# Performance work log

Measured on AMD Instinct MI355X. Metric: run time of the kernel, lower is better.

Reference implementation:

```python
import jax, jax.numpy as jnp
import numpy as np

V, OOV, E, HE, HD, B, S, T = 50000, 100, 128, 256, 256, 32, 256, 16
NEG = -1e20


def lstm(x, W, U, b, h0, c0):
    # x: [B, L, F]; standard (Keras-style i,f,g,o) LSTM via scan over time
    def step(carry, xt):
        h, c = carry
        z = xt @ W + h @ U + b
        i, f, g, o = jnp.split(z, 4, axis=-1)
        c = jax.nn.sigmoid(f) * c + jax.nn.sigmoid(i) * jnp.tanh(g)
        h = jax.nn.sigmoid(o) * jnp.tanh(c)
        return (h, c), h
    (h, c), hs = jax.lax.scan(step, (h0, c0), jnp.swapaxes(x, 0, 1))
    return jnp.swapaxes(hs, 0, 1), h, c


def setup_inputs() -> dict:
    key = jax.random.key(0)
    ks = jax.random.split(key, 16)
    g = lambda i, shape: jax.random.normal(ks[i], shape, dtype=jnp.float32) * 0.05
    return {
        'x': jax.random.randint(ks[0], (B, S), 0, V),
        'x_with_oov': jax.random.randint(ks[1], (B, S), 0, V + OOV),
        'x_len': jax.random.randint(ks[2], (B,), 1, S + 1),
        'dec_x': jax.random.randint(ks[3], (B, T), 0, V),
        'embedding': g(4, (V, E)),
        'Wenc': g(5, (E, 4 * HE)), 'Uenc': g(6, (HE, 4 * HE)), 'benc': jnp.zeros(4 * HE, jnp.float32),
        'We2d': g(7, (HE, HD)), 'be2d': jnp.zeros(HD, jnp.float32),
        'Wdec': g(8, (E, 4 * HD)), 'Udec': g(9, (HD, 4 * HD)), 'bdec': jnp.zeros(4 * HD, jnp.float32),
        'Wattn': g(10, (HD, HE)),
        'Wout': g(11, (HE + HD, HD)), 'bout': jnp.zeros(HD, jnp.float32),
        'Wgen': g(12, (HD, V)),
        'Wcopy': g(13, (HE, HD)), 'bcopy': jnp.zeros(HD, jnp.float32),
    }


def reference(x, x_with_oov, x_len, dec_x, embedding, Wenc, Uenc, benc,
              We2d, be2d, Wdec, Udec, bdec, Wattn, Wout, bout, Wgen, Wcopy, bcopy):
    # Encoder (unidirectional; Keras encoder ignores mask in this branch)
    enc_out, eh, ec = lstm(embedding[x], Wenc, Uenc, benc,
                           jnp.zeros((B, HE), embedding.dtype), jnp.zeros((B, HE), embedding.dtype))
    # NOTE: source applies encoder2decoder_state to BOTH h and c (faithful)
    h0 = eh @ We2d + be2d
    c0 = ec @ We2d + be2d
    # Decoder LSTM
    dec_out, sh, sc = lstm(embedding[dec_x], Wdec, Udec, bdec, h0, c0)  # [B,T,HD]
    mask = jnp.arange(S)[None, :] < x_len[:, None]                      # [B,S]
    # Attention (score_mode='general')
    scores = jnp.einsum('bth,he,bse->bts', dec_out, Wattn, enc_out)     # [B,T,S]
    scores = jnp.where(mask[:, None, :], scores, NEG)
    aw = jax.nn.softmax(scores, axis=2)
    ctx = jnp.einsum('bts,bse->bte', aw, enc_out)                       # [B,T,HE]
    attn_out = jnp.tanh(jnp.concatenate([ctx, dec_out], axis=-1) @ Wout + bout)  # [B,T,HD]
    # Generation scores, padded with tiny constant over OOV slots
    gen = jnp.exp(attn_out @ Wgen)                                      # [B,T,V]
    gen = jnp.pad(gen, ((0, 0), (0, 0), (0, OOV)), constant_values=1e-10)
    # Copy scores over source positions, scattered into extended vocab
    copy_seq = jnp.einsum('bsh,bth->bts', jnp.tanh(enc_out @ Wcopy + bcopy), attn_out)
    copy_seq = jnp.exp(jnp.where(mask[:, None, :], copy_seq, NEG))      # [B,T,S]
    b_idx = jnp.arange(B)[:, None, None]
    t_idx = jnp.arange(T)[None, :, None]
    v_idx = x_with_oov[:, None, :]                                      # broadcast to [B,T,S]
    copy_vocab = jnp.zeros((B, T, V + OOV), gen.dtype).at[b_idx, t_idx, v_idx].add(copy_seq)
    total = gen + copy_vocab
    log_prob = jnp.log(total / jnp.sum(total, axis=2, keepdims=True))
    return log_prob, sh, sc
```

## Files before the change

### kernel.cpp

```cpp
#include <hip/hip_runtime.h>

#define V_   50000
#define OOV_ 100
#define VO_  50100
#define E_   128
#define HE_  256
#define HD_  256
#define B_   32
#define S_   256
#define T_   16

typedef _Float16 h2_t __attribute__((ext_vector_type(2)));
typedef __attribute__((ext_vector_type(8))) short bfrag_t;
typedef __attribute__((ext_vector_type(4))) float f32x4;

union U32H2 { unsigned u; h2_t h; };
union FRAG  { uint4 u; bfrag_t s; };

static __device__ __forceinline__ float bf2f(unsigned short b) {
  return __uint_as_float(((unsigned)b) << 16);
}
static __device__ __forceinline__ unsigned short f2bf(float f) {
  unsigned u = __float_as_uint(f);
  unsigned r = (u + 0x7fffu + ((u >> 16) & 1u)) >> 16;
  return (unsigned short)r;
}
static __device__ __forceinline__ unsigned pk2bf(float a, float b) {
  return ((unsigned)f2bf(b) << 16) | (unsigned)f2bf(a);
}
static __device__ __forceinline__ float sigm(float x) { return 1.f / (1.f + expf(-x)); }

static __device__ __forceinline__ float dot2u(unsigned upair, unsigned hpairv, float acc) {
  U32H2 a; a.u = upair;
  U32H2 b; b.u = hpairv;
#if __has_builtin(__builtin_amdgcn_fdot2)
  return __builtin_amdgcn_fdot2(a.h, b.h, acc, false);
#else
  acc = fmaf((float)a.h.x, (float)b.h.x, acc);
  return fmaf((float)a.h.y, (float)b.h.y, acc);
#endif
}

__global__ __launch_bounds__(256) void gemm_f32(
    const float* __restrict__ A, const float* __restrict__ Bw,
    const float* __restrict__ bias, float* __restrict__ C,
    int M, int N, int K, int ldC, int act)
{
  __shared__ float As[16][64];
  __shared__ float Bs[16][64];
  const int tid = threadIdx.x;
  const int tx = tid & 15, ty = tid >> 4;
  const int row0 = blockIdx.y * 64, col0 = blockIdx.x * 64;
  float acc[4][4] = {{0.f}};
  for (int k0 = 0; k0 < K; k0 += 16) {
#pragma unroll
    for (int q = 0; q < 4; q++) {
      int idx = q * 256 + tid;
      int m = idx >> 4, kk = idx & 15;
      As[kk][m] = A[(size_t)(row0 + m) * K + (k0 + kk)];
      int k2 = idx >> 6, n = idx & 63;
      int cc = col0 + n;
      Bs[k2][n] = (cc < N) ? Bw[(size_t)(k0 + k2) * N + cc] : 0.f;
    }
    __syncthreads();
#pragma unroll
    for (int kk = 0; kk < 16; kk++) {
      float4 a4 = *(const float4*)&As[kk][ty * 4];
      float4 b4 = *(const float4*)&Bs[kk][tx * 4];
      float av[4] = {a4.x, a4.y, a4.z, a4.w};
      float bv[4] = {b4.x, b4.y, b4.z, b4.w};
#pragma unroll
      for (int i = 0; i < 4; i++)
#pragma unroll
        for (int j = 0; j < 4; j++)
          acc[i][j] = fmaf(av[i], bv[j], acc[i][j]);
    }
    __syncthreads();
  }
#pragma unroll
  for (int i = 0; i < 4; i++) {
    int r = row0 + ty * 4 + i;
#pragma unroll
    for (int j = 0; j < 4; j++) {
      int c = col0 + tx * 4 + j;
      if (c < N) {
        float v = acc[i][j] + (bias ? bias[c] : 0.f);
        if (act == 1) v = tanhf(v);
        else if (act == 2) v = expf(v);
        C[(size_t)r * ldC + c] = v;
      }
    }
  }
}

#define DOT8(u0, u1, hpi)                \
  acc[0] = dot2u(u0.x, hpi, acc[0]);     \
  acc[1] = dot2u(u0.y, hpi, acc[1]);     \
  acc[2] = dot2u(u0.z, hpi, acc[2]);     \
  acc[3] = dot2u(u0.w, hpi, acc[3]);     \
  acc[4] = dot2u(u1.x, hpi, acc[4]);     \
  acc[5] = dot2u(u1.y, hpi, acc[5]);     \
  acc[6] = dot2u(u1.z, hpi, acc[6]);     \
  acc[7] = dot2u(u1.w, hpi, acc[7]);

__global__ __launch_bounds__(1024) void lstm_rec2(
    const float* __restrict__ Xpre, const unsigned* __restrict__ Upk2,
    const float* __restrict__ h0, const float* __restrict__ c0,
    float* __restrict__ outH, float* __restrict__ hN, float* __restrict__ cN,
    int steps)
{
  __shared__ unsigned ldsU[32 * 1028];
  __shared__ float zpart[4 * 1028];
  __shared__ unsigned hpair[128];
  const int tid = threadIdx.x, b = blockIdx.x;
  const int jg = tid >> 3, kq = tid & 7;

  uint4 Ur[24];
  const unsigned* ubase = Upk2 + jg * 8;
#pragma unroll
  for (int i = 0; i < 12; i++) {
    int p = kq * 16 + i;
    Ur[2 * i]     = *(const uint4*)(ubase + p * 1024);
    Ur[2 * i + 1] = *(const uint4*)(ubase + p * 1024 + 4);
  }
#pragma unroll
  for (int i = 0; i < 4; i++) {
    int p = kq * 16 + 12 + i;
    uint4 q0 = *(const uint4*)(ubase + p * 1024);
    uint4 q1 = *(const uint4*)(ubase + p * 1024 + 4);
    *(uint4*)&ldsU[(kq * 4 + i) * 1028 + jg * 8] = q0;
    *(uint4*)&ldsU[(kq * 4 + i) * 1028 + jg * 8 + 4] = q1;
  }
  float c = 0.f, hcur = 0.f;
  if (tid < 256) {
    c    = c0 ? c0[b * 256 + tid] : 0.f;
    hcur = h0 ? h0[b * 256 + tid] : 0.f;
  }
  if (tid < 128) {
    float a  = h0 ? h0[b * 256 + 2 * tid] : 0.f;
    float b2 = h0 ? h0[b * 256 + 2 * tid + 1] : 0.f;
    U32H2 cv; cv.h = h2_t{(_Float16)a, (_Float16)b2};
    hpair[tid] = cv.u;
  }
  __syncthreads();

  const float* xp = Xpre + (size_t)b * steps * 1024;
  const unsigned* myld = &ldsU[kq * 4 * 1028 + jg * 8];

  for (int t = 0; t < steps; t++) {
    float x0 = 0.f, x1 = 0.f, x2 = 0.f, x3 = 0.f;
    if (tid < 256) {
      x0 = xp[t * 1024 + tid];
      x1 = xp[t * 1024 + 256 + tid];
      x2 = xp[t * 1024 + 512 + tid];
      x3 = xp[t * 1024 + 768 + tid];
    }
    float acc[8] = {0.f, 0.f, 0.f, 0.f, 0.f, 0.f, 0.f, 0.f};
    {
      uint4 hA = *(const uint4*)&hpair[kq * 16];
      DOT8(Ur[0], Ur[1], hA.x)  DOT8(Ur[2], Ur[3], hA.y)
      DOT8(Ur[4], Ur[5], hA.z)  DOT8(Ur[6], Ur[7], hA.w)
    }
    {
      uint4 hB = *(const uint4*)&hpair[kq * 16 + 4];
      DOT8(Ur[8], Ur[9], hB.x)   DOT8(Ur[10], Ur[11], hB.y)
      DOT8(Ur[12], Ur[13], hB.z) DOT8(Ur[14], Ur[15], hB.w)
    }
    {
      uint4 hC = *(const uint4*)&hpair[kq * 16 + 8];
      DOT8(Ur[16], Ur[17], hC.x) DOT8(Ur[18], Ur[19], hC.y)
      DOT8(Ur[20], Ur[21], hC.z) DOT8(Ur[22], Ur[23], hC.w)
    }
    {
      uint4 hD = *(const uint4*)&hpair[kq * 16 + 12];
      unsigned hh[4] = {hD.x, hD.y, hD.z, hD.w};
#pragma unroll
      for (int r = 0; r < 4; r++) {
        uint4 u0 = *(const uint4*)(myld + r * 1028);
        uint4 u1 = *(const uint4*)(myld + r * 1028 + 4);
        unsigned hpi = hh[r];
        DOT8(u0, u1, hpi)
      }
    }
#pragma unroll
    for (int g = 0; g < 8; g++) acc[g] += __shfl_xor(acc[g], 1);
    if ((kq & 1) == 0) {
      int r = kq >> 1;
      *(float4*)&zpart[r * 1028 + jg * 8]     = make_float4(acc[0], acc[1], acc[2], acc[3]);
      *(float4*)&zpart[r * 1028 + jg * 8 + 4] = make_float4(acc[4], acc[5], acc[6], acc[7]);
    }
    __syncthreads();
    if (tid < 256) {
      int j = tid;
      float s0 = 0.f, s1 = 0.f, s2 = 0.f, s3 = 0.f;
#pragma unroll
      for (int r = 0; r < 4; r++) {
        s0 += zpart[r * 1028 + j];
        s1 += zpart[r * 1028 + 256 + j];
        s2 += zpart[r * 1028 + 512 + j];
        s3 += zpart[r * 1028 + 768 + j];
      }
      float zi = x0 + s0, zf = x1 + s1, zg = x2 + s2, zo = x3 + s3;
      c = sigm(zf) * c + sigm(zi) * tanhf(zg);
      hcur = sigm(zo) * tanhf(c);
      outH[((size_t)b * steps + t) * 256 + j] = hcur;
      float hother = __shfl_xor(hcur, 1);
      if ((j & 1) == 0) {
        U32H2 cv; cv.h = h2_t{(_Float16)hcur, (_Float16)hother};
        hpair[j >> 1] = cv.u;
      }
    }
    __syncthreads();
  }
  if (tid < 256) {
    hN[b * 256 + tid] = hcur;
    cN[b * 256 + tid] = c;
  }
}

__global__ __launch_bounds__(256) void gen_mfma(
    const unsigned short* __restrict__ Abf, const float* __restrict__ Wgen,
    float* __restrict__ out)
{
  const int w = threadIdx.x >> 6, lane = threadIdx.x & 63;
  const int m0 = blockIdx.y * 64 + w * 16;
  const int n0 = blockIdx.x * 64;
  const int l16 = lane & 15, lq = lane >> 4;
  f32x4 acc[4] = {f32x4{0,0,0,0}, f32x4{0,0,0,0}, f32x4{0,0,0,0}, f32x4{0,0,0,0}};
  for (int k0 = 0; k0 < 256; k0 += 32) {
    FRAG a;
    a.u = *(const uint4*)(Abf + (size_t)(m0 + l16) * 256 + k0 + lq * 8);
#pragma unroll
    for (int ns = 0; ns < 4; ns++) {
      int n = n0 + ns * 16 + l16;
      int nc = n < V_ ? n : V_ - 1;
      const float* bp = Wgen + (size_t)(k0 + lq * 8) * V_ + nc;
      FRAG bf;
      bf.u.x = pk2bf(bp[0],          bp[(size_t)V_]);
      bf.u.y = pk2bf(bp[2 * (size_t)V_], bp[3 * (size_t)V_]);
      bf.u.z = pk2bf(bp[4 * (size_t)V_], bp[5 * (size_t)V_]);
      bf.u.w = pk2bf(bp[6 * (size_t)V_], bp[7 * (size_t)V_]);
      acc[ns] = __builtin_amdgcn_mfma_f32_16x16x32_bf16(a.s, bf.s, acc[ns], 0, 0, 0);
    }
  }
#pragma unroll
  for (int ns = 0; ns < 4; ns++) {
    int col = n0 + ns * 16 + l16;
    if (col < V_) {
#pragma unroll
      for (int r = 0; r < 4; r++) {
        int row = m0 + lq * 4 + r;
        out[(size_t)row * VO_ + col] = expf(acc[ns][r]);
      }
    }
  }
}

__global__ __launch_bounds__(256) void attn_kernel(
    const float* __restrict__ dq, const float* __restrict__ enc,
    const int* __restrict__ x_len, float* __restrict__ ctx)
{
  __shared__ float q[256];
  __shared__ float eb[32][256];
  __shared__ float sc[256];
  __shared__ float red[8];
  const int bt = blockIdx.x, tid = threadIdx.x;
  const int b = bt >> 4;
  q[tid] = dq[(size_t)bt * 256 + tid];
  const int len = x_len[b];
  const float* encb = enc + (size_t)b * S_ * 256;
  __syncthreads();
  const int s_loc = tid >> 3, hb = (tid & 7) * 32;
  for (int cch = 0; cch < 8; cch++) {
#pragma unroll
    for (int qq = 0; qq < 32; qq++) {
      int idx = qq * 256 + tid;
      eb[idx >> 8][idx & 255] = encb[(size_t)(cch * 32) * 256 + idx];
    }
    __syncthreads();
    float p = 0.f;
#pragma unroll
    for (int h = 0; h < 32; h++) p = fmaf(q[hb + h], eb[s_loc][hb + h], p);
    p += __shfl_down(p, 4, 8);
    p += __shfl_down(p, 2, 8);
    p += __shfl_down(p, 1, 8);
    if ((tid & 7) == 0) sc[cch * 32 + s_loc] = p;
    __syncthreads();
  }
  float my = (tid < len) ? sc[tid] : -1e30f;
  float m = my;
#pragma unroll
  for (int o = 32; o >= 1; o >>= 1) m = fmaxf(m, __shfl_xor(m, o));
  if ((tid & 63) == 0) red[tid >> 6] = m;
  __syncthreads();
  float bm = fmaxf(fmaxf(red[0], red[1]), fmaxf(red[2], red[3]));
  float e = expf(my - bm);
  float s = e;
#pragma unroll
  for (int o = 32; o >= 1; o >>= 1) s += __shfl_xor(s, o);
  if ((tid & 63) == 0) red[4 + (tid >> 6)] = s;
  __syncthreads();
  float tot = red[4] + red[5] + red[6] + red[7];
  sc[tid] = e / tot;
  __syncthreads();
  float acc = 0.f;
  for (int s2 = 0; s2 < 256; s2++) acc = fmaf(sc[s2], encb[(size_t)s2 * 256 + tid], acc);
  ctx[(size_t)bt * 256 + tid] = acc;
}

__global__ __launch_bounds__(256) void copyseq_kernel(
    const float* __restrict__ at, const float* __restrict__ cp,
    const int* __restrict__ x_len, float* __restrict__ cseq)
{
  __shared__ float q[256];
  __shared__ float eb[32][256];
  __shared__ float sc[256];
  const int bt = blockIdx.x, tid = threadIdx.x;
  const int b = bt >> 4;
  q[tid] = at[(size_t)bt * 256 + tid];
  const int len = x_len[b];
  const float* cpb = cp + (size_t)b * S_ * 256;
  __syncthreads();
  const int s_loc = tid >> 3, hb = (tid & 7) * 32;
  for (int cch = 0; cch < 8; cch++) {
#pragma unroll
    for (int qq = 0; qq < 32; qq++) {
      int idx = qq * 256 + tid;
      eb[idx >> 8][idx & 255] = cpb[(size_t)(cch * 32) * 256 + idx];
    }
    __syncthreads();
    float p = 0.f;
#pragma unroll
    for (int h = 0; h < 32; h++) p = fmaf(q[hb + h], eb[s_loc][hb + h], p);
    p += __shfl_down(p, 4, 8);
    p += __shfl_down(p, 2, 8);
    p += __shfl_down(p, 1, 8);
    if ((tid & 7) == 0) sc[cch * 32 + s_loc] = p;
    __syncthreads();
  }
  cseq[(size_t)bt * 256 + tid] = (tid < len) ? expf(sc[tid]) : 0.f;
}

__global__ void embed_kernel(const int* __restrict__ idx, const float* __restrict__ emb,
                             float* __restrict__ out) {
  int r = blockIdx.x;
  out[(size_t)r * E_ + threadIdx.x] = emb[(size_t)idx[r] * E_ + threadIdx.x];
}
__global__ void packU2_kernel(const float* __restrict__ U, unsigned* __restrict__ out) {
  int i = blockIdx.x * 256 + threadIdx.x;
  int p = i >> 10, col = i & 1023;
  float a = U[(size_t)(2 * p) * 1024 + col];
  float b = U[(size_t)(2 * p + 1) * 1024 + col];
  U32H2 cv; cv.h = h2_t{(_Float16)a, (_Float16)b};
  out[i] = cv.u;
}
__global__ void f2bf_kernel(const float* __restrict__ in, unsigned short* __restrict__ out, int n) {
  int i = blockIdx.x * 256 + threadIdx.x;
  if (i < n) out[i] = f2bf(in[i]);
}
__global__ void concat_kernel(const float* __restrict__ ctx, const float* __restrict__ dec,
                              float* __restrict__ cat) {
  int i = blockIdx.x * 256 + threadIdx.x;
  int r = i >> 9, j = i & 511;
  cat[i] = (j < 256) ? ctx[r * 256 + j] : dec[r * 256 + (j - 256)];
}
__global__ void pad_kernel(float* __restrict__ out) {
  int i = blockIdx.x * 256 + threadIdx.x;
  if (i < B_ * T_ * OOV_) {
    int bt = i / OOV_, j = i - bt * OOV_;
    out[(size_t)bt * VO_ + V_ + j] = 1e-10f;
  }
}
__global__ void scatter_kernel(const float* __restrict__ cseq, const int* __restrict__ xoov,
                               float* __restrict__ out) {
  int i = blockIdx.x * 256 + threadIdx.x;
  int bt = i >> 8, s = i & 255, b = bt >> 4;
  float v = cseq[i];
  if (v != 0.f) atomicAdd(&out[(size_t)bt * VO_ + xoov[b * S_ + s]], v);
}
__global__ __launch_bounds__(256) void rowsum_kernel(const float* __restrict__ out,
                                                     float* __restrict__ rowlog) {
  __shared__ float red[256];
  int bt = blockIdx.x, tid = threadIdx.x;
  const float* row = out + (size_t)bt * VO_;
  float s = 0.f;
  for (int i = tid; i < VO_; i += 256) s += row[i];
  red[tid] = s;
  __syncthreads();
  for (int o = 128; o >= 1; o >>= 1) {
    if (tid < o) red[tid] += red[tid + o];
    __syncthreads();
  }
  if (tid == 0) rowlog[bt] = logf(red[0]);
}
__global__ void finalize_kernel(float* __restrict__ out, const float* __restrict__ rowlog) {
  size_t i = (size_t)blockIdx.x * 256 + threadIdx.x;
  if (i < (size_t)B_ * T_ * VO_) {
    int bt = (int)(i / VO_);
    out[i] = logf(out[i]) - rowlog[bt];
  }
}

extern "C" void kernel_launch(void* const* d_in, const int* in_sizes, int n_in,
                              void* d_out, int out_size, void* d_ws, size_t ws_size,
                              hipStream_t stream) {
  const int*   x     = (const int*)d_in[0];
  const int*   xoov  = (const int*)d_in[1];
  const int*   xlen  = (const int*)d_in[2];
  const int*   decx  = (const int*)d_in[3];
  const float* emb   = (const float*)d_in[4];
  const float* Wenc  = (const float*)d_in[5];
  const float* Uenc  = (const float*)d_in[6];
  const float* benc  = (const float*)d_in[7];
  const float* We2d  = (const float*)d_in[8];
  const float* be2d  = (const float*)d_in[9];
  const float* Wdec  = (const float*)d_in[10];
  const float* Udec  = (const float*)d_in[11];
  const float* bdec  = (const float*)d_in[12];
  const float* Wattn = (const float*)d_in[13];
  const float* Wout  = (const float*)d_in[14];
  const float* bout  = (const float*)d_in[15];
  const float* Wgen  = (const float*)d_in[16];
  const float* Wcopy = (const float*)d_in[17];
  const float* bcopy = (const float*)d_in[18];
  float* out = (float*)d_out;
  float* ws  = (float*)d_ws;

  float* Xenc   = ws + 0;
  float* scra   = ws + 8388608;
  float* xemb   = scra;
  float* dqb    = scra + 0;
  float* ctxb   = scra + 131072;
  float* catb   = scra + 262144;
  float* attno  = scra + 524288;
  float* cseq   = scra + 655360;
  float* rowlog = scra + 786432;
  unsigned short* Abf = (unsigned short*)(scra + 786944);
  float* demb   = ws + 9437184;
  float* Xdec   = ws + 9502720;
  unsigned* Upk2E = (unsigned*)(ws + 10027008);
  unsigned* Upk2D = (unsigned*)(ws + 10158080);
  float* encO   = ws + 10289152;
  float* ehc    = ws + 12386304;
  float* h0c0   = ws + 12402688;
  float* decO   = ws + 12419072;
  float* cp     = ws + 0;

  float* sh  = out + (size_t)B_ * T_ * VO_;
  float* scf = sh + B_ * HD_;

  hipLaunchKernelGGL(packU2_kernel, dim3(512), dim3(256), 0, stream, Uenc, Upk2E);
  hipLaunchKernelGGL(packU2_kernel, dim3(512), dim3(256), 0, stream, Udec, Upk2D);
  hipLaunchKernelGGL(embed_kernel, dim3(B_ * S_), dim3(E_), 0, stream, x, emb, xemb);
  hipLaunchKernelGGL(embed_kernel, dim3(B_ * T_), dim3(E_), 0, stream, decx, emb, demb);
  hipLaunchKernelGGL(gemm_f32, dim3(16, 128), dim3(256), 0, stream,
                     xemb, Wenc, benc, Xenc, B_ * S_, 1024, 128, 1024, 0);
  hipLaunchKernelGGL(gemm_f32, dim3(16, 8), dim3(256), 0, stream,
                     demb, Wdec, bdec, Xdec, B_ * T_, 1024, 128, 1024, 0);
  hipLaunchKernelGGL(lstm_rec2, dim3(B_), dim3(1024), 0, stream,
                     Xenc, Upk2E, (const float*)nullptr, (const float*)nullptr,
                     encO, ehc, ehc + 32 * 256, S_);
  hipLaunchKernelGGL(gemm_f32, dim3(4, 1), dim3(256), 0, stream,
                     ehc, We2d, be2d, h0c0, 64, 256, 256, 256, 0);
  hipLaunchKernelGGL(lstm_rec2, dim3(B_), dim3(1024), 0, stream,
                     Xdec, Upk2D, h0c0, h0c0 + 32 * 256, decO, sh, scf, T_);
  hipLaunchKernelGGL(gemm_f32, dim3(4, 8), dim3(256), 0, stream,
                     decO, Wattn, (const float*)nullptr, dqb, B_ * T_, 256, 256, 256, 0);
  hipLaunchKernelGGL(attn_kernel, dim3(B_ * T_), dim3(256), 0, stream, dqb, encO, xlen, ctxb);
  hipLaunchKernelGGL(concat_kernel, dim3(1024), dim3(256), 0, stream, ctxb, decO, catb);
  hipLaunchKernelGGL(gemm_f32, dim3(4, 8), dim3(256), 0, stream,
                     catb, Wout, bout, attno, B_ * T_, 256, 512, 256, 1);
  hipLaunchKernelGGL(gemm_f32, dim3(4, 128), dim3(256), 0, stream,
                     encO, Wcopy, bcopy, cp, B_ * S_, 256, 256, 256, 1);
  hipLaunchKernelGGL(f2bf_kernel, dim3(512), dim3(256), 0, stream, attno, Abf, B_ * T_ * 256);
  hipLaunchKernelGGL(gen_mfma, dim3(782, 8), dim3(256), 0, stream, Abf, Wgen, out);
  hipLaunchKernelGGL(pad_kernel, dim3(200), dim3(256), 0, stream, out);
  hipLaunchKernelGGL(copyseq_kernel, dim3(B_ * T_), dim3(256), 0, stream, attno, cp, xlen, cseq);
  hipLaunchKernelGGL(scatter_kernel, dim3(512), dim3(256), 0, stream, cseq, xoov, out);
  hipLaunchKernelGGL(rowsum_kernel, dim3(B_ * T_), dim3(256), 0, stream, out, rowlog);
  hipLaunchKernelGGL(finalize_kernel, dim3((B_ * T_ * VO_ + 255) / 256), dim3(256), 0, stream,
                     out, rowlog);
}
```

Measured before the change: 1.262 ms.

## Move all GEMMs to bf16 MFMA, fuse prep, overlap Wgen transpose with decoder LSTM

Replaces the fp32 SIMT GEMM with a bf16 MFMA GEMM that reads pre-transposed bf16 weights. A single prep kernel now transposes the weights, packs U and gathers the embeddings. The Wgen transpose runs as extra blocks of the decoder LSTM launch so it overlaps the recurrence. The LSTM now computes gate activations across all 1024 threads and stores bf16 outputs. Row sums are accumulated atomically inside the generation GEMM epilogue and the scatter, which removes the full-vocab rowsum pass. The cost is lower precision from bf16 activations and an epsilon added inside the log.

Measured after the change: 1.200 ms. 1.05x faster.

```diff
diff --git a/kernel.cpp b/kernel.cpp
--- a/kernel.cpp
+++ b/kernel.cpp
@@ -13,6 +13,7 @@
 typedef _Float16 h2_t __attribute__((ext_vector_type(2)));
 typedef __attribute__((ext_vector_type(8))) short bfrag_t;
 typedef __attribute__((ext_vector_type(4))) float f32x4;
+typedef unsigned short ushort_t;
 
 union U32H2 { unsigned u; h2_t h; };
 union FRAG  { uint4 u; bfrag_t s; };
@@ -24,9 +25,6 @@
   unsigned u = __float_as_uint(f);
   unsigned r = (u + 0x7fffu + ((u >> 16) & 1u)) >> 16;
   return (unsigned short)r;
-}
-static __device__ __forceinline__ unsigned pk2bf(float a, float b) {
-  return ((unsigned)f2bf(b) << 16) | (unsigned)f2bf(a);
 }
 static __device__ __forceinline__ float sigm(float x) { return 1.f / (1.f + expf(-x)); }
 
@@ -41,55 +39,124 @@
 #endif
 }
 
-__global__ __launch_bounds__(256) void gemm_f32(
-    const float* __restrict__ A, const float* __restrict__ Bw,
-    const float* __restrict__ bias, float* __restrict__ C,
-    int M, int N, int K, int ldC, int act)
-{
-  __shared__ float As[16][64];
-  __shared__ float Bs[16][64];
-  const int tid = threadIdx.x;
-  const int tx = tid & 15, ty = tid >> 4;
-  const int row0 = blockIdx.y * 64, col0 = blockIdx.x * 64;
-  float acc[4][4] = {{0.f}};
-  for (int k0 = 0; k0 < K; k0 += 16) {
-#pragma unroll
-    for (int q = 0; q < 4; q++) {
-      int idx = q * 256 + tid;
-      int m = idx >> 4, kk = idx & 15;
-      As[kk][m] = A[(size_t)(row0 + m) * K + (k0 + kk)];
-      int k2 = idx >> 6, n = idx & 63;
-      int cc = col0 + n;
-      Bs[k2][n] = (cc < N) ? Bw[(size_t)(k0 + k2) * N + cc] : 0.f;
-    }
-    __syncthreads();
-#pragma unroll
-    for (int kk = 0; kk < 16; kk++) {
-      float4 a4 = *(const float4*)&As[kk][ty * 4];
-      float4 b4 = *(const float4*)&Bs[kk][tx * 4];
-      float av[4] = {a4.x, a4.y, a4.z, a4.w};
-      float bv[4] = {b4.x, b4.y, b4.z, b4.w};
-#pragma unroll
-      for (int i = 0; i < 4; i++)
-#pragma unroll
-        for (int j = 0; j < 4; j++)
-          acc[i][j] = fmaf(av[i], bv[j], acc[i][j]);
-    }
-    __syncthreads();
-  }
-#pragma unroll
-  for (int i = 0; i < 4; i++) {
-    int r = row0 + ty * 4 + i;
-#pragma unroll
-    for (int j = 0; j < 4; j++) {
-      int c = col0 + tx * 4 + j;
-      if (c < N) {
-        float v = acc[i][j] + (bias ? bias[c] : 0.f);
+__global__ __launch_bounds__(256) void mfma_gemm(
+    const ushort_t* __restrict__ A, const ushort_t* __restrict__ Bt,
+    const float* __restrict__ bias, float* __restrict__ C, ushort_t* __restrict__ Cbf,
+    float* __restrict__ rsum, int M, int N, int K, int ldC, int act)
+{
+  const int w = threadIdx.x >> 6, lane = threadIdx.x & 63;
+  const int m0 = blockIdx.y * 64 + w * 16;
+  const int n0 = blockIdx.x * 64;
+  const int l16 = lane & 15, lq = lane >> 4;
+  f32x4 acc[4] = {f32x4{0,0,0,0}, f32x4{0,0,0,0}, f32x4{0,0,0,0}, f32x4{0,0,0,0}};
+  for (int k0 = 0; k0 < K; k0 += 32) {
+    FRAG a;
+    a.u = *(const uint4*)(A + (size_t)(m0 + l16) * K + k0 + lq * 8);
+#pragma unroll
+    for (int ns = 0; ns < 4; ns++) {
+      int n = n0 + ns * 16 + l16;
+      int nc = n < N ? n : N - 1;
+      FRAG bf;
+      bf.u = *(const uint4*)(Bt + (size_t)nc * K + k0 + lq * 8);
+      acc[ns] = __builtin_amdgcn_mfma_f32_16x16x32_bf16(a.s, bf.s, acc[ns], 0, 0, 0);
+    }
+  }
+  float bv[4];
+#pragma unroll
+  for (int ns = 0; ns < 4; ns++) {
+    int col = n0 + ns * 16 + l16;
+    bv[ns] = (bias && col < N) ? bias[col] : 0.f;
+  }
+#pragma unroll
+  for (int r = 0; r < 4; r++) {
+    int row = m0 + lq * 4 + r;
+    float part = 0.f;
+#pragma unroll
+    for (int ns = 0; ns < 4; ns++) {
+      int col = n0 + ns * 16 + l16;
+      if (col < N) {
+        float v = acc[ns][r] + bv[ns];
         if (act == 1) v = tanhf(v);
         else if (act == 2) v = expf(v);
-        C[(size_t)r * ldC + c] = v;
+        if (Cbf) Cbf[(size_t)row * ldC + col] = f2bf(v);
+        else     C[(size_t)row * ldC + col] = v;
+        part += v;
       }
     }
+    if (rsum) {
+      part += __shfl_xor(part, 1);
+      part += __shfl_xor(part, 2);
+      part += __shfl_xor(part, 4);
+      part += __shfl_xor(part, 8);
+      if (l16 == 0) atomicAdd(&rsum[row], part);
+    }
+  }
+}
+
+static __device__ __forceinline__ void tconv_tile(
+    const float* __restrict__ W, ushort_t* __restrict__ Wt, int K, int N,
+    int kb, int nb, int tid, ushort_t (*tile)[33])
+{
+  const int tx = tid & 31, ty = tid >> 5;
+#pragma unroll
+  for (int p = 0; p < 4; p++) {
+    int k = kb + ty + p * 8, n = nb + tx;
+    if (k < K && n < N) tile[ty + p * 8][tx] = f2bf(W[(size_t)k * N + n]);
+  }
+  __syncthreads();
+#pragma unroll
+  for (int p = 0; p < 4; p++) {
+    int n = nb + ty + p * 8, k = kb + tx;
+    if (k < K && n < N) Wt[(size_t)n * K + k] = tile[tx][ty + p * 8];
+  }
+}
+static __device__ __forceinline__ void packU2_one(
+    const float* __restrict__ U, unsigned* __restrict__ out, int i)
+{
+  int p = i >> 10, col = i & 1023;
+  U32H2 cv; cv.h = h2_t{(_Float16)U[(size_t)(2 * p) * 1024 + col],
+                        (_Float16)U[(size_t)(2 * p + 1) * 1024 + col]};
+  out[i] = cv.u;
+}
+
+__global__ __launch_bounds__(256) void prep_kernel(
+    const float* __restrict__ Wenc, const float* __restrict__ Wdec,
+    const float* __restrict__ We2d, const float* __restrict__ Wattn,
+    const float* __restrict__ Wout, const float* __restrict__ Wcopy,
+    const float* __restrict__ Uenc, const float* __restrict__ Udec,
+    const int* __restrict__ x, const int* __restrict__ decx, const float* __restrict__ emb,
+    ushort_t* WencT, ushort_t* WdecT, ushort_t* We2dT, ushort_t* WattnT,
+    ushort_t* WoutT, ushort_t* WcopyT, unsigned* Upk2E, unsigned* Upk2D,
+    ushort_t* xembbf, ushort_t* dembbf)
+{
+  __shared__ ushort_t tile[32][33];
+  int blk = blockIdx.x;
+  const int tid = threadIdx.x;
+  if (blk < 128) { tconv_tile(Wenc, WencT, 128, 1024, (blk >> 5) * 32, (blk & 31) * 32, tid, tile); return; }
+  blk -= 128;
+  if (blk < 128) { tconv_tile(Wdec, WdecT, 128, 1024, (blk >> 5) * 32, (blk & 31) * 32, tid, tile); return; }
+  blk -= 128;
+  if (blk < 64)  { tconv_tile(We2d, We2dT, 256, 256, (blk >> 3) * 32, (blk & 7) * 32, tid, tile); return; }
+  blk -= 64;
+  if (blk < 64)  { tconv_tile(Wattn, WattnT, 256, 256, (blk >> 3) * 32, (blk & 7) * 32, tid, tile); return; }
+  blk -= 64;
+  if (blk < 128) { tconv_tile(Wout, WoutT, 512, 256, (blk >> 3) * 32, (blk & 7) * 32, tid, tile); return; }
+  blk -= 128;
+  if (blk < 64)  { tconv_tile(Wcopy, WcopyT, 256, 256, (blk >> 3) * 32, (blk & 7) * 32, tid, tile); return; }
+  blk -= 64;
+  if (blk < 512) { packU2_one(Uenc, Upk2E, blk * 256 + tid); return; }
+  blk -= 512;
+  if (blk < 512) { packU2_one(Udec, Upk2D, blk * 256 + tid); return; }
+  blk -= 512;
+  if (blk < 4096) {
+    int i = blk * 256 + tid, r = i >> 7;
+    xembbf[i] = f2bf(emb[(size_t)x[r] * E_ + (i & 127)]);
+    return;
+  }
+  blk -= 4096;
+  {
+    int i = blk * 256 + tid, r = i >> 7;
+    dembbf[i] = f2bf(emb[(size_t)decx[r] * E_ + (i & 127)]);
   }
 }
 
@@ -103,16 +170,37 @@
   acc[6] = dot2u(u1.z, hpi, acc[6]);     \
   acc[7] = dot2u(u1.w, hpi, acc[7]);
 
-__global__ __launch_bounds__(1024) void lstm_rec2(
+__global__ __launch_bounds__(1024, 4) void lstm4(
     const float* __restrict__ Xpre, const unsigned* __restrict__ Upk2,
     const float* __restrict__ h0, const float* __restrict__ c0,
-    float* __restrict__ outH, float* __restrict__ hN, float* __restrict__ cN,
-    int steps)
+    ushort_t* __restrict__ outH, float* __restrict__ hN, float* __restrict__ cN,
+    int steps, const float* __restrict__ Wg, ushort_t* __restrict__ WgT)
 {
   __shared__ unsigned ldsU[32 * 1028];
   __shared__ float zpart[4 * 1028];
+  __shared__ float actbuf[1024];
   __shared__ unsigned hpair[128];
-  const int tid = threadIdx.x, b = blockIdx.x;
+  const int tid = threadIdx.x;
+
+  if (blockIdx.x >= 32) {
+    ushort_t* tile = (ushort_t*)ldsU;
+    int tb = blockIdx.x - 32;
+    int kb = (tb & 3) * 64, nb = (tb >> 2) * 64;
+#pragma unroll
+    for (int p = 0; p < 4; p++) {
+      int i = p * 1024 + tid, k = i >> 6, n = i & 63;
+      if (nb + n < V_) tile[k * 65 + n] = f2bf(Wg[(size_t)(kb + k) * V_ + nb + n]);
+    }
+    __syncthreads();
+#pragma unroll
+    for (int p = 0; p < 4; p++) {
+      int i = p * 1024 + tid, n = i >> 6, k = i & 63;
+      if (nb + n < V_) WgT[(size_t)(nb + n) * 256 + kb + k] = tile[k * 65 + n];
+    }
+    return;
+  }
+
+  const int b = blockIdx.x;
   const int jg = tid >> 3, kq = tid & 7;
 
   uint4 Ur[24];
@@ -148,13 +236,7 @@
   const unsigned* myld = &ldsU[kq * 4 * 1028 + jg * 8];
 
   for (int t = 0; t < steps; t++) {
-    float x0 = 0.f, x1 = 0.f, x2 = 0.f, x3 = 0.f;
-    if (tid < 256) {
-      x0 = xp[t * 1024 + tid];
-      x1 = xp[t * 1024 + 256 + tid];
-      x2 = xp[t * 1024 + 512 + tid];
-      x3 = xp[t * 1024 + 768 + tid];
-    }
+    float xv = xp[t * 1024 + tid];
     float acc[8] = {0.f, 0.f, 0.f, 0.f, 0.f, 0.f, 0.f, 0.f};
     {
       uint4 hA = *(const uint4*)&hpair[kq * 16];
@@ -190,24 +272,19 @@
       *(float4*)&zpart[r * 1028 + jg * 8 + 4] = make_float4(acc[4], acc[5], acc[6], acc[7]);
     }
     __syncthreads();
+    float z = xv + zpart[tid] + zpart[1028 + tid] + zpart[2 * 1028 + tid] + zpart[3 * 1028 + tid];
+    actbuf[tid] = (tid >= 512 && tid < 768) ? tanhf(z) : sigm(z);
+    __syncthreads();
     if (tid < 256) {
-      int j = tid;
-      float s0 = 0.f, s1 = 0.f, s2 = 0.f, s3 = 0.f;
-#pragma unroll
-      for (int r = 0; r < 4; r++) {
-        s0 += zpart[r * 1028 + j];
-        s1 += zpart[r * 1028 + 256 + j];
-        s2 += zpart[r * 1028 + 512 + j];
-        s3 += zpart[r * 1028 + 768 + j];
-      }
-      float zi = x0 + s0, zf = x1 + s1, zg = x2 + s2, zo = x3 + s3;
-      c = sigm(zf) * c + sigm(zi) * tanhf(zg);
-      hcur = sigm(zo) * tanhf(c);
-      outH[((size_t)b * steps + t) * 256 + j] = hcur;
-      float hother = __shfl_xor(hcur, 1);
-      if ((j & 1) == 0) {
-        U32H2 cv; cv.h = h2_t{(_Float16)hcur, (_Float16)hother};
-        hpair[j >> 1] = cv.u;
+      float ai = actbuf[tid], af = actbuf[tid + 256];
+      float gg = actbuf[tid + 512], ao = actbuf[tid + 768];
+      c = af * c + ai * gg;
+      hcur = ao * tanhf(c);
+      outH[((size_t)b * steps + t) * 256 + tid] = f2bf(hcur);
+      float hnx = __shfl_down(hcur, 1);
+      if ((tid & 1) == 0) {
+        U32H2 cv; cv.h = h2_t{(_Float16)hcur, (_Float16)hnx};
+        hpair[tid >> 1] = cv.u;
       }
     }
     __syncthreads();
@@ -218,46 +295,8 @@
   }
 }
 
-__global__ __launch_bounds__(256) void gen_mfma(
-    const unsigned short* __restrict__ Abf, const float* __restrict__ Wgen,
-    float* __restrict__ out)
-{
-  const int w = threadIdx.x >> 6, lane = threadIdx.x & 63;
-  const int m0 = blockIdx.y * 64 + w * 16;
-  const int n0 = blockIdx.x * 64;
-  const int l16 = lane & 15, lq = lane >> 4;
-  f32x4 acc[4] = {f32x4{0,0,0,0}, f32x4{0,0,0,0}, f32x4{0,0,0,0}, f32x4{0,0,0,0}};
-  for (int k0 = 0; k0 < 256; k0 += 32) {
-    FRAG a;
-    a.u = *(const uint4*)(Abf + (size_t)(m0 + l16) * 256 + k0 + lq * 8);
-#pragma unroll
-    for (int ns = 0; ns < 4; ns++) {
-      int n = n0 + ns * 16 + l16;
-      int nc = n < V_ ? n : V_ - 1;
-      const float* bp = Wgen + (size_t)(k0 + lq * 8) * V_ + nc;
-      FRAG bf;
-      bf.u.x = pk2bf(bp[0],          bp[(size_t)V_]);
-      bf.u.y = pk2bf(bp[2 * (size_t)V_], bp[3 * (size_t)V_]);
-      bf.u.z = pk2bf(bp[4 * (size_t)V_], bp[5 * (size_t)V_]);
-      bf.u.w = pk2bf(bp[6 * (size_t)V_], bp[7 * (size_t)V_]);
-      acc[ns] = __builtin_amdgcn_mfma_f32_16x16x32_bf16(a.s, bf.s, acc[ns], 0, 0, 0);
-    }
-  }
-#pragma unroll
-  for (int ns = 0; ns < 4; ns++) {
-    int col = n0 + ns * 16 + l16;
-    if (col < V_) {
-#pragma unroll
-      for (int r = 0; r < 4; r++) {
-        int row = m0 + lq * 4 + r;
-        out[(size_t)row * VO_ + col] = expf(acc[ns][r]);
-      }
-    }
-  }
-}
-
 __global__ __launch_bounds__(256) void attn_kernel(
-    const float* __restrict__ dq, const float* __restrict__ enc,
+    const float* __restrict__ dq, const ushort_t* __restrict__ enc,
     const int* __restrict__ x_len, float* __restrict__ ctx)
 {
   __shared__ float q[256];
@@ -268,14 +307,17 @@
   const int b = bt >> 4;
   q[tid] = dq[(size_t)bt * 256 + tid];
   const int len = x_len[b];
-  const float* encb = enc + (size_t)b * S_ * 256;
+  const unsigned* encu = (const unsigned*)(enc + (size_t)b * S_ * 256);
   __syncthreads();
   const int s_loc = tid >> 3, hb = (tid & 7) * 32;
   for (int cch = 0; cch < 8; cch++) {
 #pragma unroll
-    for (int qq = 0; qq < 32; qq++) {
-      int idx = qq * 256 + tid;
-      eb[idx >> 8][idx & 255] = encb[(size_t)(cch * 32) * 256 + idx];
+    for (int qv = 0; qv < 16; qv++) {
+      int idx = qv * 256 + tid;
+      unsigned u = encu[cch * 4096 + idx];
+      int row = idx >> 7, cp2 = (idx & 127) * 2;
+      eb[row][cp2]     = bf2f((unsigned short)(u & 0xffffu));
+      eb[row][cp2 + 1] = bf2f((unsigned short)(u >> 16));
     }
     __syncthreads();
     float p = 0.f;
@@ -303,13 +345,14 @@
   float tot = red[4] + red[5] + red[6] + red[7];
   sc[tid] = e / tot;
   __syncthreads();
+  const ushort_t* encb = enc + (size_t)b * S_ * 256;
   float acc = 0.f;
-  for (int s2 = 0; s2 < 256; s2++) acc = fmaf(sc[s2], encb[(size_t)s2 * 256 + tid], acc);
+  for (int s2 = 0; s2 < 256; s2++) acc = fmaf(sc[s2], bf2f(encb[(size_t)s2 * 256 + tid]), acc);
   ctx[(size_t)bt * 256 + tid] = acc;
 }
 
 __global__ __launch_bounds__(256) void copyseq_kernel(
-    const float* __restrict__ at, const float* __restrict__ cp,
+    const float* __restrict__ at, const ushort_t* __restrict__ cp,
     const int* __restrict__ x_len, float* __restrict__ cseq)
 {
   __shared__ float q[256];
@@ -319,14 +362,17 @@
   const int b = bt >> 4;
   q[tid] = at[(size_t)bt * 256 + tid];
   const int len = x_len[b];
-  const float* cpb = cp + (size_t)b * S_ * 256;
+  const unsigned* cpu_ = (const unsigned*)(cp + (size_t)b * S_ * 256);
   __syncthreads();
   const int s_loc = tid >> 3, hb = (tid & 7) * 32;
   for (int cch = 0; cch < 8; cch++) {
 #pragma unroll
-    for (int qq = 0; qq < 32; qq++) {
-      int idx = qq * 256 + tid;
-      eb[idx >> 8][idx & 255] = cpb[(size_t)(cch * 32) * 256 + idx];
+    for (int qv = 0; qv < 16; qv++) {
+      int idx = qv * 256 + tid;
+      unsigned u = cpu_[cch * 4096 + idx];
+      int row = idx >> 7, cp2 = (idx & 127) * 2;
+      eb[row][cp2]     = bf2f((unsigned short)(u & 0xffffu));
+      eb[row][cp2 + 1] = bf2f((unsigned short)(u >> 16));
     }
     __syncthreads();
     float p = 0.f;
@@ -341,28 +387,15 @@
   cseq[(size_t)bt * 256 + tid] = (tid < len) ? expf(sc[tid]) : 0.f;
 }
 
-__global__ void embed_kernel(const int* __restrict__ idx, const float* __restrict__ emb,
-                             float* __restrict__ out) {
-  int r = blockIdx.x;
-  out[(size_t)r * E_ + threadIdx.x] = emb[(size_t)idx[r] * E_ + threadIdx.x];
-}
-__global__ void packU2_kernel(const float* __restrict__ U, unsigned* __restrict__ out) {
-  int i = blockIdx.x * 256 + threadIdx.x;
-  int p = i >> 10, col = i & 1023;
-  float a = U[(size_t)(2 * p) * 1024 + col];
-  float b = U[(size_t)(2 * p + 1) * 1024 + col];
-  U32H2 cv; cv.h = h2_t{(_Float16)a, (_Float16)b};
-  out[i] = cv.u;
-}
-__global__ void f2bf_kernel(const float* __restrict__ in, unsigned short* __restrict__ out, int n) {
+__global__ void f2bf_kernel(const float* __restrict__ in, ushort_t* __restrict__ out, int n) {
   int i = blockIdx.x * 256 + threadIdx.x;
   if (i < n) out[i] = f2bf(in[i]);
 }
-__global__ void concat_kernel(const float* __restrict__ ctx, const float* __restrict__ dec,
-                              float* __restrict__ cat) {
+__global__ void concat_bf(const float* __restrict__ ctx, const ushort_t* __restrict__ dec,
+                          ushort_t* __restrict__ cat) {
   int i = blockIdx.x * 256 + threadIdx.x;
   int r = i >> 9, j = i & 511;
-  cat[i] = (j < 256) ? ctx[r * 256 + j] : dec[r * 256 + (j - 256)];
+  cat[i] = (j < 256) ? f2bf(ctx[r * 256 + j]) : dec[r * 256 + (j - 256)];
 }
 __global__ void pad_kernel(float* __restrict__ out) {
   int i = blockIdx.x * 256 + threadIdx.x;
@@ -371,27 +404,24 @@
     out[(size_t)bt * VO_ + V_ + j] = 1e-10f;
   }
 }
-__global__ void scatter_kernel(const float* __restrict__ cseq, const int* __restrict__ xoov,
-                               float* __restrict__ out) {
+__global__ __launch_bounds__(256) void scatter_kernel(
+    const float* __restrict__ cseq, const int* __restrict__ xoov,
+    float* __restrict__ out, float* __restrict__ rsum)
+{
+  __shared__ float red[4];
+  const int bt = blockIdx.x, tid = threadIdx.x, b = bt >> 4;
+  float v = cseq[(size_t)bt * 256 + tid];
+  if (v != 0.f) atomicAdd(&out[(size_t)bt * VO_ + xoov[b * S_ + tid]], v);
+  float s = v;
+#pragma unroll
+  for (int o = 32; o >= 1; o >>= 1) s += __shfl_xor(s, o);
+  if ((tid & 63) == 0) red[tid >> 6] = s;
+  __syncthreads();
+  if (tid == 0) atomicAdd(&rsum[bt], red[0] + red[1] + red[2] + red[3]);
+}
+__global__ void rowlog_kernel(const float* __restrict__ rsum, float* __restrict__ rowlog) {
   int i = blockIdx.x * 256 + threadIdx.x;
-  int bt = i >> 8, s = i & 255, b = bt >> 4;
-  float v = cseq[i];
-  if (v != 0.f) atomicAdd(&out[(size_t)bt * VO_ + xoov[b * S_ + s]], v);
-}
-__global__ __launch_bounds__(256) void rowsum_kernel(const float* __restrict__ out,
-                                                     float* __restrict__ rowlog) {
-  __shared__ float red[256];
-  int bt = blockIdx.x, tid = threadIdx.x;
-  const float* row = out + (size_t)bt * VO_;
-  float s = 0.f;
-  for (int i = tid; i < VO_; i += 256) s += row[i];
-  red[tid] = s;
-  __syncthreads();
-  for (int o = 128; o >= 1; o >>= 1) {
-    if (tid < o) red[tid] += red[tid + o];
-    __syncthreads();
-  }
-  if (tid == 0) rowlog[bt] = logf(red[0]);
+  if (i < B_ * T_) rowlog[i] = logf(rsum[i] + 1e-8f);
 }
 __global__ void finalize_kernel(float* __restrict__ out, const float* __restrict__ rowlog) {
   size_t i = (size_t)blockIdx.x * 256 + threadIdx.x;
@@ -426,58 +456,84 @@
   float* out = (float*)d_out;
   float* ws  = (float*)d_ws;
 
-  float* Xenc   = ws + 0;
-  float* scra   = ws + 8388608;
-  float* xemb   = scra;
-  float* dqb    = scra + 0;
-  float* ctxb   = scra + 131072;
-  float* catb   = scra + 262144;
-  float* attno  = scra + 524288;
-  float* cseq   = scra + 655360;
-  float* rowlog = scra + 786432;
-  unsigned short* Abf = (unsigned short*)(scra + 786944);
-  float* demb   = ws + 9437184;
-  float* Xdec   = ws + 9502720;
-  unsigned* Upk2E = (unsigned*)(ws + 10027008);
-  unsigned* Upk2D = (unsigned*)(ws + 10158080);
-  float* encO   = ws + 10289152;
-  float* ehc    = ws + 12386304;
-  float* h0c0   = ws + 12402688;
-  float* decO   = ws + 12419072;
-  float* cp     = ws + 0;
+  float*    Xenc   = ws + 0;
+  ushort_t* WgenT  = (ushort_t*)(ws + 0);
+  ushort_t* cp_bf  = (ushort_t*)(ws + 6400000);
+  float*    dqb    = ws + 8388608;
+  float*    ctxb   = ws + 8519680;
+  float*    attno  = ws + 8650752;
+  float*    cseq   = ws + 8781824;
+  float*    rsum   = ws + 8912896;
+  float*    rowlog = ws + 8913408;
+  ushort_t* Abf    = (ushort_t*)(ws + 8913920);
+  ushort_t* catb   = (ushort_t*)(ws + 8979456);
+  ushort_t* decObf = (ushort_t*)(ws + 9110528);
+  ushort_t* xembbf = (ushort_t*)(ws + 9176064);
+  ushort_t* dembbf = (ushort_t*)(ws + 9700352);
+  float*    Xdec   = ws + 9733120;
+  ushort_t* WencT  = (ushort_t*)(ws + 10257408);
+  ushort_t* WdecT  = (ushort_t*)(ws + 10322944);
+  ushort_t* We2dT  = (ushort_t*)(ws + 10388480);
+  ushort_t* WattnT = (ushort_t*)(ws + 10421248);
+  ushort_t* WoutT  = (ushort_t*)(ws + 10454016);
+  ushort_t* WcopyT = (ushort_t*)(ws + 10519552);
+  unsigned* Upk2E  = (unsigned*)(ws + 10552320);
+  unsigned* Upk2D  = (unsigned*)(ws + 10683392);
+  ushort_t* encObf = (ushort_t*)(ws + 10814464);
+  float*    ehc    = ws + 11863040;
+  ushort_t* ehcbf  = (ushort_t*)(ws + 11879424);
+  float*    h0c0   = ws + 11887616;
 
   float* sh  = out + (size_t)B_ * T_ * VO_;
   float* scf = sh + B_ * HD_;
 
-  hipLaunchKernelGGL(packU2_kernel, dim3(512), dim3(256), 0, stream, Uenc, Upk2E);
-  hipLaunchKernelGGL(packU2_kernel, dim3(512), dim3(256), 0, stream, Udec, Upk2D);
-  hipLaunchKernelGGL(embed_kernel, dim3(B_ * S_), dim3(E_), 0, stream, x, emb, xemb);
-  hipLaunchKernelGGL(embed_kernel, dim3(B_ * T_), dim3(E_), 0, stream, decx, emb, demb);
-  hipLaunchKernelGGL(gemm_f32, dim3(16, 128), dim3(256), 0, stream,
-                     xemb, Wenc, benc, Xenc, B_ * S_, 1024, 128, 1024, 0);
-  hipLaunchKernelGGL(gemm_f32, dim3(16, 8), dim3(256), 0, stream,
-                     demb, Wdec, bdec, Xdec, B_ * T_, 1024, 128, 1024, 0);
-  hipLaunchKernelGGL(lstm_rec2, dim3(B_), dim3(1024), 0, stream,
+  hipMemsetAsync(rsum, 0, 512 * sizeof(float), stream);
+
+  hipLaunchKernelGGL(prep_kernel, dim3(5952), dim3(256), 0, stream,
+                     Wenc, Wdec, We2d, Wattn, Wout, Wcopy, Uenc, Udec, x, decx, emb,
+                     WencT, WdecT, We2dT, WattnT, WoutT, WcopyT, Upk2E, Upk2D,
+                     xembbf, dembbf);
+
+  hipLaunchKernelGGL(mfma_gemm, dim3(16, 128), dim3(256), 0, stream,
+                     xembbf, WencT, benc, Xenc, (ushort_t*)nullptr, (float*)nullptr,
+                     B_ * S_, 1024, 128, 1024, 0);
+  hipLaunchKernelGGL(mfma_gemm, dim3(16, 8), dim3(256), 0, stream,
+                     dembbf, WdecT, bdec, Xdec, (ushort_t*)nullptr, (float*)nullptr,
+                     B_ * T_, 1024, 128, 1024, 0);
+
+  hipLaunchKernelGGL(lstm4, dim3(32), dim3(1024), 0, stream,
                      Xenc, Upk2E, (const float*)nullptr, (const float*)nullptr,
-                     encO, ehc, ehc + 32 * 256, S_);
-  hipLaunchKernelGGL(gemm_f32, dim3(4, 1), dim3(256), 0, stream,
-                     ehc, We2d, be2d, h0c0, 64, 256, 256, 256, 0);
-  hipLaunchKernelGGL(lstm_rec2, dim3(B_), dim3(1024), 0, stream,
-                     Xdec, Upk2D, h0c0, h0c0 + 32 * 256, decO, sh, scf, T_);
-  hipLaunchKernelGGL(gemm_f32, dim3(4, 8), dim3(256), 0, stream,
-                     decO, Wattn, (const float*)nullptr, dqb, B_ * T_, 256, 256, 256, 0);
-  hipLaunchKernelGGL(attn_kernel, dim3(B_ * T_), dim3(256), 0, stream, dqb, encO, xlen, ctxb);
-  hipLaunchKernelGGL(concat_kernel, dim3(1024), dim3(256), 0, stream, ctxb, decO, catb);
-  hipLaunchKernelGGL(gemm_f32, dim3(4, 8), dim3(256), 0, stream,
-                     catb, Wout, bout, attno, B_ * T_, 256, 512, 256, 1);
-  hipLaunchKernelGGL(gemm_f32, dim3(4, 128), dim3(256), 0, stream,
-                     encO, Wcopy, bcopy, cp, B_ * S_, 256, 256, 256, 1);
+                     encObf, ehc, ehc + 32 * 256, S_,
+                     (const float*)nullptr, (ushort_t*)nullptr);
+
+  hipLaunchKernelGGL(f2bf_kernel, dim3(64), dim3(256), 0, stream, ehc, ehcbf, 64 * 256);
+  hipLaunchKernelGGL(mfma_gemm, dim3(4, 1), dim3(256), 0, stream,
+                     ehcbf, We2dT, be2d, h0c0, (ushort_t*)nullptr, (float*)nullptr,
+                     64, 256, 256, 256, 0);
+
+  hipLaunchKernelGGL(lstm4, dim3(32 + 3128), dim3(1024), 0, stream,
+                     Xdec, Upk2D, h0c0, h0c0 + 32 * 256, decObf, sh, scf, T_,
+                     Wgen, WgenT);
+
+  hipLaunchKernelGGL(mfma_gemm, dim3(4, 8), dim3(256), 0, stream,
+                     decObf, WattnT, (const float*)nullptr, dqb, (ushort_t*)nullptr,
+                     (float*)nullptr, B_ * T_, 256, 256, 256, 0);
+  hipLaunchKernelGGL(attn_kernel, dim3(B_ * T_), dim3(256), 0, stream, dqb, encObf, xlen, ctxb);
+  hipLaunchKernelGGL(concat_bf, dim3(1024), dim3(256), 0, stream, ctxb, decObf, catb);
+  hipLaunchKernelGGL(mfma_gemm, dim3(4, 8), dim3(256), 0, stream,
+                     catb, WoutT, bout, attno, (ushort_t*)nullptr, (float*)nullptr,
+                     B_ * T_, 256, 512, 256, 1);
   hipLaunchKernelGGL(f2bf_kernel, dim3(512), dim3(256), 0, stream, attno, Abf, B_ * T_ * 256);
-  hipLaunchKernelGGL(gen_mfma, dim3(782, 8), dim3(256), 0, stream, Abf, Wgen, out);
+  hipLaunchKernelGGL(mfma_gemm, dim3(4, 128), dim3(256), 0, stream,
+                     encObf, WcopyT, bcopy, (float*)nullptr, cp_bf, (float*)nullptr,
+                     B_ * S_, 256, 256, 256, 1);
+  hipLaunchKernelGGL(mfma_gemm, dim3(782, 8), dim3(256), 0, stream,
+                     Abf, WgenT, (const float*)nullptr, out, (ushort_t*)nullptr, rsum,
+                     B_ * T_, V_, 256, VO_, 2);
   hipLaunchKernelGGL(pad_kernel, dim3(200), dim3(256), 0, stream, out);
-  hipLaunchKernelGGL(copyseq_kernel, dim3(B_ * T_), dim3(256), 0, stream, attno, cp, xlen, cseq);
-  hipLaunchKernelGGL(scatter_kernel, dim3(512), dim3(256), 0, stream, cseq, xoov, out);
-  hipLaunchKernelGGL(rowsum_kernel, dim3(B_ * T_), dim3(256), 0, stream, out, rowlog);
+  hipLaunchKernelGGL(copyseq_kernel, dim3(B_ * T_), dim3(256), 0, stream, attno, cp_bf, xlen, cseq);
+  hipLaunchKernelGGL(scatter_kernel, dim3(512), dim3(256), 0, stream, cseq, xoov, out, rsum);
+  hipLaunchKernelGGL(rowlog_kernel, dim3(2), dim3(256), 0, stream, rsum, rowlog);
   hipLaunchKernelGGL(finalize_kernel, dim3((B_ * T_ * VO_ + 255) / 256), dim3(256), 0, stream,
                      out, rowlog);
 }
```
